# Kernel tuning notes

Hardware: AMD Instinct MI355X
Metric: run time of the kernel (lower is better)

The kernel has to match this reference:

```python
import jax, jax.numpy as jnp
import numpy as np
import math

CHUNK_SIZE = 1024

def setup_inputs() -> dict:
    key = jax.random.key(0)
    kq, kk, kv = jax.random.split(key, 3)
    B, H, T, D = 2, 16, 4096, 128
    return {
        "query": jax.random.normal(kq, (B, H, T, D), dtype=jnp.float32),
        "key": jax.random.normal(kk, (B, H, T, D), dtype=jnp.float32),
        "value": jax.random.normal(kv, (B, H, T, D), dtype=jnp.float32),
    }

def _chunked_causal_attention(query, key, value, chunk_size=CHUNK_SIZE):
    B, H, T, D = query.shape
    scale = 1.0 / math.sqrt(D)
    num_chunks = (T + chunk_size - 1) // chunk_size
    outputs = []
    for ci in range(num_chunks):
        start = ci * chunk_size
        end = min((ci + 1) * chunk_size, T)
        q_chunk = query[:, :, start:end, :]            # [B,H,c,D]
        k_chunk = key[:, :, :end, :]                   # [B,H,end,D]
        v_chunk = value[:, :, :end, :]                 # [B,H,end,D]
        scores = jnp.einsum('bhqd,bhkd->bhqk', q_chunk, k_chunk) * scale
        # causal mask: key position must be <= query position
        q_idx = jnp.arange(start, end)[:, None]        # [c,1]
        k_idx = jnp.arange(end)[None, :]               # [1,end]
        scores = jnp.where(k_idx <= q_idx, scores, -jnp.inf)
        weights = jax.nn.softmax(scores, axis=-1)
        outputs.append(jnp.einsum('bhqk,bhkd->bhqd', weights, v_chunk))
    return jnp.concatenate(outputs, axis=2)

def reference(query, key, value):
    return _chunked_causal_attention(query, key, value)
```

## Files before the change

### kernel.cpp

```cpp
#include <hip/hip_runtime.h>
#include <stdint.h>


typedef __bf16 bf16x8 __attribute__((ext_vector_type(8)));
typedef float f32x16 __attribute__((ext_vector_type(16)));
typedef unsigned short u16x8 __attribute__((ext_vector_type(8)));
typedef unsigned int u32x2 __attribute__((ext_vector_type(2)));

#define T_SEQ 4096
#define D_HEAD 128
#define BQ 128
#define BK 64
#define KSTR 136
#define VSTR 72

__device__ __forceinline__ unsigned int pack_bf2(float a, float b) {
    unsigned int ua = __builtin_bit_cast(unsigned int, a) + 0x8000u;
    unsigned int ub = __builtin_bit_cast(unsigned int, b) + 0x8000u;
    return __builtin_amdgcn_perm(ub, ua, 0x07060302);
}

__global__ __launch_bounds__(256, 2) void fa_fwd(
    const float* __restrict__ Qg, const float* __restrict__ Kg,
    const float* __restrict__ Vg, float* __restrict__ Og)
{
    __shared__ unsigned short K_lds[BK * KSTR];
    __shared__ unsigned short Vt_lds[D_HEAD * VSTR];

    const int tid  = threadIdx.x;
    const int w    = tid >> 6;
    const int lane = tid & 63;
    const int r    = lane & 31;
    const int h    = lane >> 5;

    const int qt = (int)(gridDim.x - 1 - blockIdx.x);
    const int bh = blockIdx.y;
    const int q0 = qt * BQ;

    const float* Qb = Qg + (size_t)bh * T_SEQ * D_HEAD;
    const float* Kb = Kg + (size_t)bh * T_SEQ * D_HEAD;
    const float* Vb = Vg + (size_t)bh * T_SEQ * D_HEAD;
    float*       Ob = Og + (size_t)bh * T_SEQ * D_HEAD;

    const int qw      = q0 + 32 * w;
    const int q_lane  = qw + r;
    const int qw_last = qw + 31;

    const float qscale = 0.08838834764831845f * 1.4426950408889634f;
    bf16x8 qf[8];
#pragma unroll
    for (int c = 0; c < 8; ++c) {
        const float* src = Qb + (size_t)q_lane * D_HEAD + c * 16 + h * 8;
        float4 f0 = *(const float4*)(src);
        float4 f1 = *(const float4*)(src + 4);
        unsigned int u0 = pack_bf2(f0.x * qscale, f0.y * qscale);
        unsigned int u1 = pack_bf2(f0.z * qscale, f0.w * qscale);
        unsigned int u2 = pack_bf2(f1.x * qscale, f1.y * qscale);
        unsigned int u3 = pack_bf2(f1.z * qscale, f1.w * qscale);
        u16x8 u = { (unsigned short)u0, (unsigned short)(u0 >> 16),
                    (unsigned short)u1, (unsigned short)(u1 >> 16),
                    (unsigned short)u2, (unsigned short)(u2 >> 16),
                    (unsigned short)u3, (unsigned short)(u3 >> 16) };
        qf[c] = __builtin_bit_cast(bf16x8, u);
    }

    f32x16 o[4];
#pragma unroll
    for (int mt = 0; mt < 4; ++mt) o[mt] = (f32x16)0.0f;
    float m_run = -1e30f, l_run = 0.0f;

    const int krow = tid >> 5;
    const int kd0  = (tid & 31) * 4;
    const int vd   = tid & 127;
    const int vhh  = tid >> 7;

    float4 kpre[8];
    float  vpre[8][4];

#pragma unroll
    for (int p = 0; p < 8; ++p)
        kpre[p] = *(const float4*)(Kb + (size_t)(p * 8 + krow) * D_HEAD + kd0);
#pragma unroll
    for (int p = 0; p < 8; ++p) {
        const int kv0 = p * 8 + vhh * 4;
        const float* vs = Vb + (size_t)kv0 * D_HEAD + vd;
        vpre[p][0] = vs[0];
        vpre[p][1] = vs[D_HEAD];
        vpre[p][2] = vs[2 * D_HEAD];
        vpre[p][3] = vs[3 * D_HEAD];
    }

    const int ntiles = 2 * qt + 2;
    for (int kt = 0; kt < ntiles; ++kt) {
        const int kbase = kt * BK;
        __syncthreads();

#pragma unroll
        for (int p = 0; p < 8; ++p) {
            u32x2 u;
            u[0] = pack_bf2(kpre[p].x, kpre[p].y);
            u[1] = pack_bf2(kpre[p].z, kpre[p].w);
            *(u32x2*)&K_lds[(p * 8 + krow) * KSTR + kd0] = u;
        }
#pragma unroll
        for (int p = 0; p < 8; ++p) {
            u32x2 u;
            u[0] = pack_bf2(vpre[p][0], vpre[p][1]);
            u[1] = pack_bf2(vpre[p][2], vpre[p][3]);
            const int col = (p >> 1) * 16 + vhh * 8 + (p & 1) * 4;
            *(u32x2*)&Vt_lds[vd * VSTR + col] = u;
        }
        __syncthreads();

        if (kt + 1 < ntiles) {
            const int nb = kbase + BK;
#pragma unroll
            for (int p = 0; p < 8; ++p)
                kpre[p] = *(const float4*)(Kb + (size_t)(nb + p * 8 + krow) * D_HEAD + kd0);
#pragma unroll
            for (int p = 0; p < 8; ++p) {
                const int kv0 = nb + p * 8 + vhh * 4;
                const float* vs = Vb + (size_t)kv0 * D_HEAD + vd;
                vpre[p][0] = vs[0];
                vpre[p][1] = vs[D_HEAD];
                vpre[p][2] = vs[2 * D_HEAD];
                vpre[p][3] = vs[3 * D_HEAD];
            }
        }

        if (kbase > qw_last) continue;

        f32x16 s[2];
        s[0] = (f32x16)0.0f; s[1] = (f32x16)0.0f;
        __builtin_amdgcn_s_setprio(1);
#pragma unroll
        for (int t = 0; t < 2; ++t) {
#pragma unroll
            for (int c = 0; c < 8; ++c) {
                u16x8 raw = *(const u16x8*)&K_lds[(t * 32 + r) * KSTR + c * 16 + h * 8];
                bf16x8 a = __builtin_bit_cast(bf16x8, raw);
                s[t] = __builtin_amdgcn_mfma_f32_32x32x16_bf16(a, qf[c], s[t], 0, 0, 0);
            }
        }
        __builtin_amdgcn_s_setprio(0);

        if (kbase + BK - 1 > qw) {
#pragma unroll
            for (int t = 0; t < 2; ++t)
#pragma unroll
                for (int g = 0; g < 16; ++g) {
                    int kv = kbase + t * 32 + (g & 3) + 8 * (g >> 2) + 4 * h;
                    if (kv > q_lane) s[t][g] = -1e30f;
                }
        }

        float mloc = -1e30f;
#pragma unroll
        for (int t = 0; t < 2; ++t)
#pragma unroll
            for (int g = 0; g < 16; ++g) mloc = fmaxf(mloc, s[t][g]);
        mloc = fmaxf(mloc, __shfl_xor(mloc, 32, 64));

        if (!__all(mloc - m_run <= 8.0f)) {
            const float m_new = fmaxf(m_run, mloc);
            const float alpha = __builtin_amdgcn_exp2f(m_run - m_new);
            l_run *= alpha;
#pragma unroll
            for (int mt = 0; mt < 4; ++mt)
#pragma unroll
                for (int g = 0; g < 16; ++g) o[mt][g] *= alpha;
            m_run = m_new;
        }

        float rsum = 0.0f;
#pragma unroll
        for (int t = 0; t < 2; ++t)
#pragma unroll
            for (int g = 0; g < 16; ++g) {
                float p = __builtin_amdgcn_exp2f(s[t][g] - m_run);
                s[t][g] = p;
                rsum += p;
            }
        rsum += __shfl_xor(rsum, 32, 64);
        l_run += rsum;

        bf16x8 pf[4];
#pragma unroll
        for (int c = 0; c < 4; ++c) {
            const int t  = c >> 1;
            const int g0 = (c & 1) * 8;
            unsigned int u0 = pack_bf2(s[t][g0 + 0], s[t][g0 + 1]);
            unsigned int u1 = pack_bf2(s[t][g0 + 2], s[t][g0 + 3]);
            unsigned int u2 = pack_bf2(s[t][g0 + 4], s[t][g0 + 5]);
            unsigned int u3 = pack_bf2(s[t][g0 + 6], s[t][g0 + 7]);
            u16x8 u = { (unsigned short)u0, (unsigned short)(u0 >> 16),
                        (unsigned short)u1, (unsigned short)(u1 >> 16),
                        (unsigned short)u2, (unsigned short)(u2 >> 16),
                        (unsigned short)u3, (unsigned short)(u3 >> 16) };
            pf[c] = __builtin_bit_cast(bf16x8, u);
        }

        __builtin_amdgcn_s_setprio(1);
#pragma unroll
        for (int mt = 0; mt < 4; ++mt) {
#pragma unroll
            for (int c = 0; c < 4; ++c) {
                u16x8 raw = *(const u16x8*)&Vt_lds[(mt * 32 + r) * VSTR + c * 16 + h * 8];
                bf16x8 a = __builtin_bit_cast(bf16x8, raw);
                o[mt] = __builtin_amdgcn_mfma_f32_32x32x16_bf16(a, pf[c], o[mt], 0, 0, 0);
            }
        }
        __builtin_amdgcn_s_setprio(0);
    }

    const float inv = 1.0f / l_run;
#pragma unroll
    for (int mt = 0; mt < 4; ++mt)
#pragma unroll
        for (int g4 = 0; g4 < 4; ++g4) {
            float4 vv;
            vv.x = o[mt][g4 * 4 + 0] * inv;
            vv.y = o[mt][g4 * 4 + 1] * inv;
            vv.z = o[mt][g4 * 4 + 2] * inv;
            vv.w = o[mt][g4 * 4 + 3] * inv;
            const int dd = mt * 32 + g4 * 8 + h * 4;
            *(float4*)(Ob + (size_t)q_lane * D_HEAD + dd) = vv;
        }
}

extern "C" void kernel_launch(void* const* d_in, const int* in_sizes, int n_in,
                              void* d_out, int out_size, void* d_ws, size_t ws_size,
                              hipStream_t stream) {
    const float* Q = (const float*)d_in[0];
    const float* K = (const float*)d_in[1];
    const float* V = (const float*)d_in[2];
    float* O = (float*)d_out;
    const int BH = in_sizes[0] / (T_SEQ * D_HEAD);
    dim3 grid(T_SEQ / BQ, BH, 1);
    fa_fwd<<<grid, 256, 0, stream>>>(Q, K, V, O);
}
```

Measured before the change: 496.2 us.

## Remap blocks to a 1D grid with balanced causal tile ordering and raise occupancy hint

Flattens the grid to 1D and remaps block IDs so that each wave of 256 blocks covers all 32 heads with query tiles taken in a zigzag order (long, short, mid-long, mid-short), so that causal work is balanced across dispatch waves. It also raises the launch-bounds occupancy hint from 2 to 4 blocks per CU, which caps register use and may force spills given the large accumulator footprint. The grid size is now hardcoded to 32 batch-heads instead of being derived from input sizes.

New measurement: 1.464 ms. 195% more time.

```diff
diff --git a/kernel.cpp b/kernel.cpp
--- a/kernel.cpp
+++ b/kernel.cpp
@@ -10,6 +10,7 @@
 #define T_SEQ 4096
 #define D_HEAD 128
 #define BQ 128
+#define NQT (T_SEQ / BQ)
 #define BK 64
 #define KSTR 136
 #define VSTR 72
@@ -20,7 +21,7 @@
     return __builtin_amdgcn_perm(ub, ua, 0x07060302);
 }
 
-__global__ __launch_bounds__(256, 2) void fa_fwd(
+__global__ __launch_bounds__(256, 4) void fa_fwd(
     const float* __restrict__ Qg, const float* __restrict__ Kg,
     const float* __restrict__ Vg, float* __restrict__ Og)
 {
@@ -33,9 +34,13 @@
     const int r    = lane & 31;
     const int h    = lane >> 5;
 
-    const int qt = (int)(gridDim.x - 1 - blockIdx.x);
-    const int bh = blockIdx.y;
-    const int q0 = qt * BQ;
+    const int bid = (int)blockIdx.x;
+    const int g   = bid & 255;
+    const int j   = bid >> 8;
+    const int t   = g & 7;
+    const int bh  = g >> 3;
+    const int qt  = (j == 0) ? (31 - t) : (j == 1) ? t : (j == 2) ? (16 + t) : (15 - t);
+    const int q0  = qt * BQ;
 
     const float* Qb = Qg + (size_t)bh * T_SEQ * D_HEAD;
     const float* Kb = Kg + (size_t)bh * T_SEQ * D_HEAD;
@@ -134,31 +139,31 @@
         s[0] = (f32x16)0.0f; s[1] = (f32x16)0.0f;
         __builtin_amdgcn_s_setprio(1);
 #pragma unroll
-        for (int t = 0; t < 2; ++t) {
+        for (int t2 = 0; t2 < 2; ++t2) {
 #pragma unroll
             for (int c = 0; c < 8; ++c) {
-                u16x8 raw = *(const u16x8*)&K_lds[(t * 32 + r) * KSTR + c * 16 + h * 8];
+                u16x8 raw = *(const u16x8*)&K_lds[(t2 * 32 + r) * KSTR + c * 16 + h * 8];
                 bf16x8 a = __builtin_bit_cast(bf16x8, raw);
-                s[t] = __builtin_amdgcn_mfma_f32_32x32x16_bf16(a, qf[c], s[t], 0, 0, 0);
+                s[t2] = __builtin_amdgcn_mfma_f32_32x32x16_bf16(a, qf[c], s[t2], 0, 0, 0);
             }
         }
         __builtin_amdgcn_s_setprio(0);
 
         if (kbase + BK - 1 > qw) {
 #pragma unroll
-            for (int t = 0; t < 2; ++t)
-#pragma unroll
-                for (int g = 0; g < 16; ++g) {
-                    int kv = kbase + t * 32 + (g & 3) + 8 * (g >> 2) + 4 * h;
-                    if (kv > q_lane) s[t][g] = -1e30f;
+            for (int t2 = 0; t2 < 2; ++t2)
+#pragma unroll
+                for (int g2 = 0; g2 < 16; ++g2) {
+                    int kv = kbase + t2 * 32 + (g2 & 3) + 8 * (g2 >> 2) + 4 * h;
+                    if (kv > q_lane) s[t2][g2] = -1e30f;
                 }
         }
 
         float mloc = -1e30f;
 #pragma unroll
-        for (int t = 0; t < 2; ++t)
-#pragma unroll
-            for (int g = 0; g < 16; ++g) mloc = fmaxf(mloc, s[t][g]);
+        for (int t2 = 0; t2 < 2; ++t2)
+#pragma unroll
+            for (int g2 = 0; g2 < 16; ++g2) mloc = fmaxf(mloc, s[t2][g2]);
         mloc = fmaxf(mloc, __shfl_xor(mloc, 32, 64));
 
         if (!__all(mloc - m_run <= 8.0f)) {
@@ -168,17 +173,17 @@
 #pragma unroll
             for (int mt = 0; mt < 4; ++mt)
 #pragma unroll
-                for (int g = 0; g < 16; ++g) o[mt][g] *= alpha;
+                for (int g2 = 0; g2 < 16; ++g2) o[mt][g2] *= alpha;
             m_run = m_new;
         }
 
         float rsum = 0.0f;
 #pragma unroll
-        for (int t = 0; t < 2; ++t)
-#pragma unroll
-            for (int g = 0; g < 16; ++g) {
-                float p = __builtin_amdgcn_exp2f(s[t][g] - m_run);
-                s[t][g] = p;
+        for (int t2 = 0; t2 < 2; ++t2)
+#pragma unroll
+            for (int g2 = 0; g2 < 16; ++g2) {
+                float p = __builtin_amdgcn_exp2f(s[t2][g2] - m_run);
+                s[t2][g2] = p;
                 rsum += p;
             }
         rsum += __shfl_xor(rsum, 32, 64);
@@ -187,12 +192,12 @@
         bf16x8 pf[4];
 #pragma unroll
         for (int c = 0; c < 4; ++c) {
-            const int t  = c >> 1;
+            const int tt = c >> 1;
             const int g0 = (c & 1) * 8;
-            unsigned int u0 = pack_bf2(s[t][g0 + 0], s[t][g0 + 1]);
-            unsigned int u1 = pack_bf2(s[t][g0 + 2], s[t][g0 + 3]);
-            unsigned int u2 = pack_bf2(s[t][g0 + 4], s[t][g0 + 5]);
-            unsigned int u3 = pack_bf2(s[t][g0 + 6], s[t][g0 + 7]);
+            unsigned int u0 = pack_bf2(s[tt][g0 + 0], s[tt][g0 + 1]);
+            unsigned int u1 = pack_bf2(s[tt][g0 + 2], s[tt][g0 + 3]);
+            unsigned int u2 = pack_bf2(s[tt][g0 + 4], s[tt][g0 + 5]);
+            unsigned int u3 = pack_bf2(s[tt][g0 + 6], s[tt][g0 + 7]);
             u16x8 u = { (unsigned short)u0, (unsigned short)(u0 >> 16),
                         (unsigned short)u1, (unsigned short)(u1 >> 16),
                         (unsigned short)u2, (unsigned short)(u2 >> 16),
@@ -235,7 +240,6 @@
     const float* K = (const float*)d_in[1];
     const float* V = (const float*)d_in[2];
     float* O = (float*)d_out;
-    const int BH = in_sizes[0] / (T_SEQ * D_HEAD);
-    dim3 grid(T_SEQ / BQ, BH, 1);
+    dim3 grid(NQT * 32, 1, 1);
     fa_fwd<<<grid, 256, 0, stream>>>(Q, K, V, O);
 }
```
